# Kernel tuning notes

Hardware: AMD Instinct MI355X
Metric: run time of the kernel (lower is better)

Reference implementation:

```python
import jax, jax.numpy as jnp
import numpy as np


def setup_inputs() -> dict:
    key = jax.random.key(0)
    k1, k2 = jax.random.split(key)
    T, D, K = 100000, 768, 500  # frames, feature dim (HuBERT base), k-means clusters
    feat = jax.random.normal(k1, (T, D), dtype=jnp.float32)
    C = jax.random.normal(k2, (D, K), dtype=jnp.float32)  # cluster centers, transposed as in module
    return {"feat": feat, "C": C}


def reference(feat, C):
    # Squared euclidean distance expanded: ||f||^2 - 2 f.C + ||c||^2
    Cnorm = jnp.sum(C * C, axis=0, keepdims=True)            # [1, K]
    fnorm = jnp.sum(feat * feat, axis=1, keepdims=True)       # [T, 1]
    dist = fnorm - 2.0 * jnp.matmul(feat, C) + Cnorm          # [T, K]
    return jnp.argmin(dist, axis=1)[None, :]                  # [1, T] cluster ids
```

## Files before the change

kernel.cpp:

```cpp
#include <hip/hip_runtime.h>
#include <float.h>

#define D_DIM 768
#define K_DIM 500
#define NDT   24
#define BM    64
#define NTH   256
#define PB_STRIDE 100352

typedef _Float16 f16x8 __attribute__((ext_vector_type(8)));
typedef float    f32x4 __attribute__((ext_vector_type(4)));


__global__ void cnorm_partial_kernel(const float* __restrict__ C,
                                     double* __restrict__ partial, int K) {
    const int k = threadIdx.x;
    const int w = blockIdx.x;
    double s = 0.0;
    if (k < K) {
        const int d0 = w * (D_DIM / 16);
        for (int d = d0; d < d0 + (D_DIM / 16); ++d) {
            const float c = C[(size_t)d * K + k];
            s = fma((double)c, (double)c, s);
        }
    }
    partial[w * 512 + k] = s;
}

__global__ void cnorm_finish_kernel(const double* __restrict__ partial,
                                    float* __restrict__ cnorm, int K) {
    const int k = threadIdx.x;
    if (k < K) {
        double s = 0.0;
        for (int w = 0; w < 16; ++w) s += partial[w * 512 + k];
        cnorm[k] = (float)s;
    } else {
        cnorm[k] = FLT_MAX;
    }
}

__global__ void packB_kernel(const float* __restrict__ C,
                             _Float16* __restrict__ BpH,
                             _Float16* __restrict__ BpL) {
    const int idx = blockIdx.x * 256 + threadIdx.x;
    const int col = idx & 511;
    const int dt  = idx >> 9;
    f16x8 h[4], l[4];
    #pragma unroll
    for (int c = 0; c < 4; ++c)
        #pragma unroll
        for (int j = 0; j < 8; ++j) {
            const int k = c * 8 + j;
            const float v = (col < K_DIM)
                          ? C[(size_t)(dt * 32 + k) * K_DIM + col] : 0.0f;
            const _Float16 hh = (_Float16)v;
            h[c][j] = hh;
            l[c][j] = (_Float16)(v - (float)hh);
        }
    f16x8* dH = (f16x8*)(BpH + ((size_t)dt * 512 + col) * 32);
    f16x8* dL = (f16x8*)(BpL + ((size_t)dt * 512 + col) * 32);
    #pragma unroll
    for (int c = 0; c < 4; ++c) { dH[c] = h[c]; dL[c] = l[c]; }
}

__launch_bounds__(NTH, 3)
__global__ void assign_kernel(const float* __restrict__ feat,
                              const _Float16* __restrict__ BpH,
                              const _Float16* __restrict__ BpL,
                              const float* __restrict__ cnorm,
                              float* __restrict__ pbv,
                              int* __restrict__ pbi,
                              int T) {
    __shared__ __align__(16) _Float16 AsH[2][BM * 32];
    __shared__ __align__(16) _Float16 AsL[2][BM * 32];
    __shared__ float red_v[BM * 4];
    __shared__ int   red_i[BM * 4];

    const int tid  = threadIdx.x;
    const int wn   = tid >> 6;
    const int lane = tid & 63;
    const int l15  = lane & 15;
    const int kg   = lane >> 4;
    const int bid  = blockIdx.x;
    const int half = bid & 1;
    const int R0   = (bid >> 1) * BM;

    const int ar = tid >> 2;
    const int ac = (tid & 3) << 3;
    const bool arow_ok = (R0 + ar) < T;
    const float* fptr = feat + (size_t)(R0 + ar) * D_DIM + ac;
    const int asl = ((ac >> 3) + (ar >> 1)) & 3;

    const int colbase = half * 256 + wn * 64 + l15;
    const _Float16* bpH = BpH + (size_t)colbase * 32 + kg * 8;
    const _Float16* bpL = BpL + (size_t)colbase * 32 + kg * 8;

    f32x4 acc[4][4];
    #pragma unroll
    for (int m = 0; m < 4; ++m)
        #pragma unroll
        for (int n = 0; n < 4; ++n) acc[m][n] = (f32x4){0.f, 0.f, 0.f, 0.f};

    {
        float4 v0 = make_float4(0.f, 0.f, 0.f, 0.f), v1 = v0;
        if (arow_ok) {
            v0 = *(const float4*)(fptr);
            v1 = *(const float4*)(fptr + 4);
        }
        const float fa[8] = {v0.x, v0.y, v0.z, v0.w, v1.x, v1.y, v1.z, v1.w};
        f16x8 h, l;
        #pragma unroll
        for (int j = 0; j < 8; ++j) {
            const _Float16 hh = (_Float16)fa[j];
            h[j] = hh; l[j] = (_Float16)(fa[j] - (float)hh);
        }
        ((f16x8*)AsH[0])[ar * 4 + asl] = h;
        ((f16x8*)AsL[0])[ar * 4 + asl] = l;
    }
    __syncthreads();

    for (int dt = 0; dt < NDT; ++dt) {
        const int cur = dt & 1;
        const bool hasNext = (dt + 1) < NDT;

        f16x8 aH[4], aL[4];
        #pragma unroll
        for (int m = 0; m < 4; ++m) {
            const int row = m * 16 + l15;
            const int sl  = (kg + (row >> 1)) & 3;
            aH[m] = ((const f16x8*)AsH[cur])[row * 4 + sl];
            aL[m] = ((const f16x8*)AsL[cur])[row * 4 + sl];
        }

        const size_t bo = (size_t)dt * 16384;
        f16x8 bH[4], bL[4];
        #pragma unroll
        for (int nh = 0; nh < 4; ++nh) {
            bH[nh] = *(const f16x8*)(bpH + bo + nh * 512);
            bL[nh] = *(const f16x8*)(bpL + bo + nh * 512);
        }

        float4 v0 = make_float4(0.f, 0.f, 0.f, 0.f), v1 = v0;
        if (hasNext && arow_ok) {
            v0 = *(const float4*)(fptr + (dt + 1) * 32);
            v1 = *(const float4*)(fptr + (dt + 1) * 32 + 4);
        }

        #pragma unroll
        for (int nh = 0; nh < 4; ++nh) {
            #pragma unroll
            for (int m = 0; m < 4; ++m) {
                f32x4 a = acc[m][nh];
                a = __builtin_amdgcn_mfma_f32_16x16x32_f16(aH[m], bH[nh], a, 0, 0, 0);
                a = __builtin_amdgcn_mfma_f32_16x16x32_f16(aL[m], bH[nh], a, 0, 0, 0);
                a = __builtin_amdgcn_mfma_f32_16x16x32_f16(aH[m], bL[nh], a, 0, 0, 0);
                acc[m][nh] = a;
            }
        }

        if (hasNext) {
            const float fa[8] = {v0.x, v0.y, v0.z, v0.w, v1.x, v1.y, v1.z, v1.w};
            f16x8 h, l;
            #pragma unroll
            for (int j = 0; j < 8; ++j) {
                const _Float16 hh = (_Float16)fa[j];
                h[j] = hh; l[j] = (_Float16)(fa[j] - (float)hh);
            }
            ((f16x8*)AsH[cur ^ 1])[ar * 4 + asl] = h;
            ((f16x8*)AsL[cur ^ 1])[ar * 4 + asl] = l;
        }
        __syncthreads();
    }

    float cn[4];
    #pragma unroll
    for (int nh = 0; nh < 4; ++nh)
        cn[nh] = cnorm[half * 256 + wn * 64 + nh * 16 + l15];

    #pragma unroll
    for (int m = 0; m < 4; ++m) {
        #pragma unroll
        for (int r = 0; r < 4; ++r) {
            float best = cn[0] - 2.0f * acc[m][0][r];
            int   bi   = colbase;
            #pragma unroll
            for (int nh = 1; nh < 4; ++nh) {
                const int col = colbase + nh * 16;
                const float s = cn[nh] - 2.0f * acc[m][nh][r];
                if (s < best || (s == best && col < bi)) { best = s; bi = col; }
            }
            #pragma unroll
            for (int msk = 1; msk < 16; msk <<= 1) {
                const float ov = __shfl_xor(best, msk, 64);
                const int   oi = __shfl_xor(bi,   msk, 64);
                if (ov < best || (ov == best && oi < bi)) { best = ov; bi = oi; }
            }
            if (l15 == 0) {
                const int rl = m * 16 + kg * 4 + r;
                red_v[rl * 4 + wn] = best;
                red_i[rl * 4 + wn] = bi;
            }
        }
    }
    __syncthreads();

    if (tid < BM) {
        float bv = red_v[tid * 4];
        int   bi = red_i[tid * 4];
        #pragma unroll
        for (int w = 1; w < 4; ++w) {
            const float v = red_v[tid * 4 + w];
            const int   i = red_i[tid * 4 + w];
            if (v < bv || (v == bv && i < bi)) { bv = v; bi = i; }
        }
        const int r = R0 + tid;
        if (r < T) {
            pbv[(size_t)half * PB_STRIDE + r] = bv;
            pbi[(size_t)half * PB_STRIDE + r] = bi;
        }
    }
}

__global__ void combine_kernel(const float* __restrict__ pbv,
                               const int* __restrict__ pbi,
                               int* __restrict__ out, int T) {
    const int r = blockIdx.x * 256 + threadIdx.x;
    if (r < T) {
        const float s0 = pbv[r];
        const int   i0 = pbi[r];
        const float s1 = pbv[PB_STRIDE + r];
        const int   i1 = pbi[PB_STRIDE + r];
        out[r] = (s1 < s0) ? i1 : i0;
    }
}

extern "C" void kernel_launch(void* const* d_in, const int* in_sizes, int n_in,
                              void* d_out, int out_size, void* d_ws, size_t ws_size,
                              hipStream_t stream) {
    const float* feat = (const float*)d_in[0];
    const float* C    = (const float*)d_in[1];
    int* out          = (int*)d_out;
    const int T = in_sizes[0] / D_DIM;
    const int K = in_sizes[1] / D_DIM;

    float*     cnorm   = (float*)d_ws;
    double*    partial = (double*)((char*)d_ws + 4096);
    _Float16*  BpH     = (_Float16*)((char*)d_ws + 131072);
    _Float16*  BpL     = (_Float16*)((char*)d_ws + 917504);
    float*     pbv     = (float*)((char*)d_ws + 1703936);
    int*       pbi     = (int*)((char*)d_ws + 2506752);

    hipLaunchKernelGGL(cnorm_partial_kernel, dim3(16), dim3(512), 0, stream,
                       C, partial, K);
    hipLaunchKernelGGL(cnorm_finish_kernel, dim3(1), dim3(512), 0, stream,
                       partial, cnorm, K);
    hipLaunchKernelGGL(packB_kernel, dim3(48), dim3(256), 0, stream,
                       C, BpH, BpL);

    const int nrb = (T + BM - 1) / BM;
    hipLaunchKernelGGL(assign_kernel, dim3(nrb * 2), dim3(NTH), 0, stream,
                       feat, BpH, BpL, cnorm, pbv, pbi, T);
    hipLaunchKernelGGL(combine_kernel, dim3((T + 255) / 256), dim3(256), 0, stream,
                       pbv, pbi, out, T);
}
```

Baseline: 272.2 us.

## Switch split-fp16 GEMM to 32x32x16 MFMA tiles with raised issue priority

Replaces the 16x16x32 MFMA tiling (4x4 accumulators of 4 floats) with 32x32x16 MFMA tiles (2x2 accumulators of 16 floats) and remaps the LDS A-fragment and global B-fragment loads to match the new operand layout. The larger tiles need fewer LDS and global fragment loads per FLOP and fewer MFMA instructions. The argmin epilogue is rewritten for the 32-lane column layout and the new output row mapping. s_setprio is raised around the MFMA block to favour matrix-instruction issue across waves. The change risks register pressure at 3 waves per SIMD and depends on the row-index remapping being correct.

```diff
diff --git a/kernel.cpp b/kernel.cpp
--- a/kernel.cpp
+++ b/kernel.cpp
@@ -8,8 +8,8 @@
 #define NTH   256
 #define PB_STRIDE 100352
 
-typedef _Float16 f16x8 __attribute__((ext_vector_type(8)));
-typedef float    f32x4 __attribute__((ext_vector_type(4)));
+typedef _Float16 f16x8  __attribute__((ext_vector_type(8)));
+typedef float    f32x16 __attribute__((ext_vector_type(16)));
 
 
 __global__ void cnorm_partial_kernel(const float* __restrict__ C,
@@ -79,8 +79,8 @@
     const int tid  = threadIdx.x;
     const int wn   = tid >> 6;
     const int lane = tid & 63;
-    const int l15  = lane & 15;
-    const int kg   = lane >> 4;
+    const int c5   = lane & 31;
+    const int kh   = lane >> 5;
     const int bid  = blockIdx.x;
     const int half = bid & 1;
     const int R0   = (bid >> 1) * BM;
@@ -91,15 +91,17 @@
     const float* fptr = feat + (size_t)(R0 + ar) * D_DIM + ac;
     const int asl = ((ac >> 3) + (ar >> 1)) & 3;
 
-    const int colbase = half * 256 + wn * 64 + l15;
-    const _Float16* bpH = BpH + (size_t)colbase * 32 + kg * 8;
-    const _Float16* bpL = BpL + (size_t)colbase * 32 + kg * 8;
-
-    f32x4 acc[4][4];
-    #pragma unroll
-    for (int m = 0; m < 4; ++m)
-        #pragma unroll
-        for (int n = 0; n < 4; ++n) acc[m][n] = (f32x4){0.f, 0.f, 0.f, 0.f};
+    const int colbase = half * 256 + wn * 64 + c5;
+    const _Float16* bpH = BpH + (size_t)colbase * 32 + kh * 8;
+    const _Float16* bpL = BpL + (size_t)colbase * 32 + kh * 8;
+
+    f32x16 acc[2][2];
+    #pragma unroll
+    for (int m = 0; m < 2; ++m)
+        #pragma unroll
+        for (int n = 0; n < 2; ++n)
+            #pragma unroll
+            for (int r = 0; r < 16; ++r) acc[m][n][r] = 0.0f;
 
     {
         float4 v0 = make_float4(0.f, 0.f, 0.f, 0.f), v1 = v0;
@@ -123,22 +125,15 @@
         const int cur = dt & 1;
         const bool hasNext = (dt + 1) < NDT;
 
-        f16x8 aH[4], aL[4];
-        #pragma unroll
-        for (int m = 0; m < 4; ++m) {
-            const int row = m * 16 + l15;
-            const int sl  = (kg + (row >> 1)) & 3;
-            aH[m] = ((const f16x8*)AsH[cur])[row * 4 + sl];
-            aL[m] = ((const f16x8*)AsL[cur])[row * 4 + sl];
-        }
-
         const size_t bo = (size_t)dt * 16384;
-        f16x8 bH[4], bL[4];
-        #pragma unroll
-        for (int nh = 0; nh < 4; ++nh) {
-            bH[nh] = *(const f16x8*)(bpH + bo + nh * 512);
-            bL[nh] = *(const f16x8*)(bpL + bo + nh * 512);
-        }
+        f16x8 bH[2][2], bL[2][2];
+        #pragma unroll
+        for (int n = 0; n < 2; ++n)
+            #pragma unroll
+            for (int step = 0; step < 2; ++step) {
+                bH[n][step] = *(const f16x8*)(bpH + bo + n * 1024 + step * 16);
+                bL[n][step] = *(const f16x8*)(bpL + bo + n * 1024 + step * 16);
+            }
 
         float4 v0 = make_float4(0.f, 0.f, 0.f, 0.f), v1 = v0;
         if (hasNext && arow_ok) {
@@ -146,17 +141,33 @@
             v1 = *(const float4*)(fptr + (dt + 1) * 32 + 4);
         }
 
-        #pragma unroll
-        for (int nh = 0; nh < 4; ++nh) {
-            #pragma unroll
-            for (int m = 0; m < 4; ++m) {
-                f32x4 a = acc[m][nh];
-                a = __builtin_amdgcn_mfma_f32_16x16x32_f16(aH[m], bH[nh], a, 0, 0, 0);
-                a = __builtin_amdgcn_mfma_f32_16x16x32_f16(aL[m], bH[nh], a, 0, 0, 0);
-                a = __builtin_amdgcn_mfma_f32_16x16x32_f16(aH[m], bL[nh], a, 0, 0, 0);
-                acc[m][nh] = a;
-            }
-        }
+        f16x8 aH[2][2], aL[2][2];
+        #pragma unroll
+        for (int m = 0; m < 2; ++m) {
+            const int row = m * 32 + c5;
+            #pragma unroll
+            for (int step = 0; step < 2; ++step) {
+                const int chunk = step * 2 + kh;
+                const int sl = (chunk + (row >> 1)) & 3;
+                aH[m][step] = ((const f16x8*)AsH[cur])[row * 4 + sl];
+                aL[m][step] = ((const f16x8*)AsL[cur])[row * 4 + sl];
+            }
+        }
+
+        __builtin_amdgcn_s_setprio(1);
+        #pragma unroll
+        for (int step = 0; step < 2; ++step)
+            #pragma unroll
+            for (int n = 0; n < 2; ++n)
+                #pragma unroll
+                for (int m = 0; m < 2; ++m) {
+                    f32x16 a = acc[m][n];
+                    a = __builtin_amdgcn_mfma_f32_32x32x16_f16(aH[m][step], bH[n][step], a, 0, 0, 0);
+                    a = __builtin_amdgcn_mfma_f32_32x32x16_f16(aL[m][step], bH[n][step], a, 0, 0, 0);
+                    a = __builtin_amdgcn_mfma_f32_32x32x16_f16(aH[m][step], bL[n][step], a, 0, 0, 0);
+                    acc[m][n] = a;
+                }
+        __builtin_amdgcn_s_setprio(0);
 
         if (hasNext) {
             const float fa[8] = {v0.x, v0.y, v0.z, v0.w, v1.x, v1.y, v1.z, v1.w};
@@ -172,31 +183,30 @@
         __syncthreads();
     }
 
-    float cn[4];
-    #pragma unroll
-    for (int nh = 0; nh < 4; ++nh)
-        cn[nh] = cnorm[half * 256 + wn * 64 + nh * 16 + l15];
-
-    #pragma unroll
-    for (int m = 0; m < 4; ++m) {
-        #pragma unroll
-        for (int r = 0; r < 4; ++r) {
+    float cn[2];
+    #pragma unroll
+    for (int n = 0; n < 2; ++n)
+        cn[n] = cnorm[half * 256 + wn * 64 + n * 32 + c5];
+
+    #pragma unroll
+    for (int m = 0; m < 2; ++m) {
+        #pragma unroll
+        for (int r = 0; r < 16; ++r) {
             float best = cn[0] - 2.0f * acc[m][0][r];
             int   bi   = colbase;
-            #pragma unroll
-            for (int nh = 1; nh < 4; ++nh) {
-                const int col = colbase + nh * 16;
-                const float s = cn[nh] - 2.0f * acc[m][nh][r];
-                if (s < best || (s == best && col < bi)) { best = s; bi = col; }
-            }
-            #pragma unroll
-            for (int msk = 1; msk < 16; msk <<= 1) {
+            {
+                const float s = cn[1] - 2.0f * acc[m][1][r];
+                const int col = colbase + 32;
+                if (s < best) { best = s; bi = col; }
+            }
+            #pragma unroll
+            for (int msk = 1; msk < 32; msk <<= 1) {
                 const float ov = __shfl_xor(best, msk, 64);
                 const int   oi = __shfl_xor(bi,   msk, 64);
                 if (ov < best || (ov == best && oi < bi)) { best = ov; bi = oi; }
             }
-            if (l15 == 0) {
-                const int rl = m * 16 + kg * 4 + r;
+            if (c5 == 0) {
+                const int rl = m * 32 + 4 * kh + (r & 3) + 8 * (r >> 2);
                 red_v[rl * 4 + wn] = best;
                 red_i[rl * 4 + wn] = bi;
             }
```

New measurement: 326.3 us. +19.9%, slower.

## Process two K-slices per loop iteration and raise MFMA wave priority

Applied to the files above, without the earlier changes.

The main loop now covers two 32-wide depth slices per iteration, so there are 12 iterations instead of 24. This halves the number of __syncthreads barriers and issues more global loads before the MFMA work starts. The MFMA blocks are wrapped in s_setprio so waves in their matrix phase are favoured by the scheduler. In exchange, LDS use and the register load from the extra B fragments both roughly double, which may cut occupancy under launch_bounds(256,3).

```diff
diff --git a/kernel.cpp b/kernel.cpp
--- a/kernel.cpp
+++ b/kernel.cpp
@@ -3,7 +3,7 @@
 
 #define D_DIM 768
 #define K_DIM 500
-#define NDT   24
+#define NIT   12
 #define BM    64
 #define NTH   256
 #define PB_STRIDE 100352
@@ -71,8 +71,8 @@
                               float* __restrict__ pbv,
                               int* __restrict__ pbi,
                               int T) {
-    __shared__ __align__(16) _Float16 AsH[2][BM * 32];
-    __shared__ __align__(16) _Float16 AsL[2][BM * 32];
+    __shared__ __align__(16) _Float16 AsH[2][2][BM * 32];
+    __shared__ __align__(16) _Float16 AsL[2][2][BM * 32];
     __shared__ float red_v[BM * 4];
     __shared__ int   red_i[BM * 4];
 
@@ -101,76 +101,112 @@
         #pragma unroll
         for (int n = 0; n < 4; ++n) acc[m][n] = (f32x4){0.f, 0.f, 0.f, 0.f};
 
+#define CVT_STORE(V0, V1, BUF, SUB) do {                                       \
+    const float fa[8] = {(V0).x, (V0).y, (V0).z, (V0).w,                       \
+                         (V1).x, (V1).y, (V1).z, (V1).w};                      \
+    f16x8 h, l;                                                                \
+    _Pragma("unroll")                                                          \
+    for (int j = 0; j < 8; ++j) {                                              \
+        const _Float16 hh = (_Float16)fa[j];                                   \
+        h[j] = hh; l[j] = (_Float16)(fa[j] - (float)hh);                       \
+    }                                                                          \
+    ((f16x8*)AsH[BUF][SUB])[ar * 4 + asl] = h;                                 \
+    ((f16x8*)AsL[BUF][SUB])[ar * 4 + asl] = l;                                 \
+} while (0)
+
     {
-        float4 v0 = make_float4(0.f, 0.f, 0.f, 0.f), v1 = v0;
+        float4 v0 = make_float4(0.f,0.f,0.f,0.f), v1 = v0, v2 = v0, v3 = v0;
         if (arow_ok) {
             v0 = *(const float4*)(fptr);
             v1 = *(const float4*)(fptr + 4);
-        }
-        const float fa[8] = {v0.x, v0.y, v0.z, v0.w, v1.x, v1.y, v1.z, v1.w};
-        f16x8 h, l;
-        #pragma unroll
-        for (int j = 0; j < 8; ++j) {
-            const _Float16 hh = (_Float16)fa[j];
-            h[j] = hh; l[j] = (_Float16)(fa[j] - (float)hh);
-        }
-        ((f16x8*)AsH[0])[ar * 4 + asl] = h;
-        ((f16x8*)AsL[0])[ar * 4 + asl] = l;
+            v2 = *(const float4*)(fptr + 32);
+            v3 = *(const float4*)(fptr + 36);
+        }
+        CVT_STORE(v0, v1, 0, 0);
+        CVT_STORE(v2, v3, 0, 1);
     }
     __syncthreads();
 
-    for (int dt = 0; dt < NDT; ++dt) {
-        const int cur = dt & 1;
-        const bool hasNext = (dt + 1) < NDT;
-
-        f16x8 aH[4], aL[4];
-        #pragma unroll
-        for (int m = 0; m < 4; ++m) {
-            const int row = m * 16 + l15;
-            const int sl  = (kg + (row >> 1)) & 3;
-            aH[m] = ((const f16x8*)AsH[cur])[row * 4 + sl];
-            aL[m] = ((const f16x8*)AsL[cur])[row * 4 + sl];
-        }
-
-        const size_t bo = (size_t)dt * 16384;
-        f16x8 bH[4], bL[4];
+    for (int it = 0; it < NIT; ++it) {
+        const int cur = it & 1;
+        const bool hasNext = (it + 1) < NIT;
+
+        const size_t bo0 = (size_t)(2 * it) * 16384;
+        const size_t bo1 = bo0 + 16384;
+        f16x8 b0H[4], b0L[4], b1H[4], b1L[4];
         #pragma unroll
         for (int nh = 0; nh < 4; ++nh) {
-            bH[nh] = *(const f16x8*)(bpH + bo + nh * 512);
-            bL[nh] = *(const f16x8*)(bpL + bo + nh * 512);
-        }
-
-        float4 v0 = make_float4(0.f, 0.f, 0.f, 0.f), v1 = v0;
+            b0H[nh] = *(const f16x8*)(bpH + bo0 + nh * 512);
+            b0L[nh] = *(const f16x8*)(bpL + bo0 + nh * 512);
+        }
+        #pragma unroll
+        for (int nh = 0; nh < 4; ++nh) {
+            b1H[nh] = *(const f16x8*)(bpH + bo1 + nh * 512);
+            b1L[nh] = *(const f16x8*)(bpL + bo1 + nh * 512);
+        }
+
+        float4 v0 = make_float4(0.f,0.f,0.f,0.f), v1 = v0, v2 = v0, v3 = v0;
         if (hasNext && arow_ok) {
-            v0 = *(const float4*)(fptr + (dt + 1) * 32);
-            v1 = *(const float4*)(fptr + (dt + 1) * 32 + 4);
-        }
-
-        #pragma unroll
-        for (int nh = 0; nh < 4; ++nh) {
+            const float* p = fptr + (it + 1) * 64;
+            v0 = *(const float4*)(p);
+            v1 = *(const float4*)(p + 4);
+            v2 = *(const float4*)(p + 32);
+            v3 = *(const float4*)(p + 36);
+        }
+
+        {
+            f16x8 aH[4], aL[4];
             #pragma unroll
             for (int m = 0; m < 4; ++m) {
-                f32x4 a = acc[m][nh];
-                a = __builtin_amdgcn_mfma_f32_16x16x32_f16(aH[m], bH[nh], a, 0, 0, 0);
-                a = __builtin_amdgcn_mfma_f32_16x16x32_f16(aL[m], bH[nh], a, 0, 0, 0);
-                a = __builtin_amdgcn_mfma_f32_16x16x32_f16(aH[m], bL[nh], a, 0, 0, 0);
-                acc[m][nh] = a;
-            }
+                const int row = m * 16 + l15;
+                const int sl  = (kg + (row >> 1)) & 3;
+                aH[m] = ((const f16x8*)AsH[cur][0])[row * 4 + sl];
+                aL[m] = ((const f16x8*)AsL[cur][0])[row * 4 + sl];
+            }
+            __builtin_amdgcn_s_setprio(1);
+            #pragma unroll
+            for (int nh = 0; nh < 4; ++nh)
+                #pragma unroll
+                for (int m = 0; m < 4; ++m) {
+                    f32x4 a = acc[m][nh];
+                    a = __builtin_amdgcn_mfma_f32_16x16x32_f16(aH[m], b0H[nh], a, 0, 0, 0);
+                    a = __builtin_amdgcn_mfma_f32_16x16x32_f16(aL[m], b0H[nh], a, 0, 0, 0);
+                    a = __builtin_amdgcn_mfma_f32_16x16x32_f16(aH[m], b0L[nh], a, 0, 0, 0);
+                    acc[m][nh] = a;
+                }
+            __builtin_amdgcn_s_setprio(0);
+        }
+
+        {
+            f16x8 aH[4], aL[4];
+            #pragma unroll
+            for (int m = 0; m < 4; ++m) {
+                const int row = m * 16 + l15;
+                const int sl  = (kg + (row >> 1)) & 3;
+                aH[m] = ((const f16x8*)AsH[cur][1])[row * 4 + sl];
+                aL[m] = ((const f16x8*)AsL[cur][1])[row * 4 + sl];
+            }
+            __builtin_amdgcn_s_setprio(1);
+            #pragma unroll
+            for (int nh = 0; nh < 4; ++nh)
+                #pragma unroll
+                for (int m = 0; m < 4; ++m) {
+                    f32x4 a = acc[m][nh];
+                    a = __builtin_amdgcn_mfma_f32_16x16x32_f16(aH[m], b1H[nh], a, 0, 0, 0);
+                    a = __builtin_amdgcn_mfma_f32_16x16x32_f16(aL[m], b1H[nh], a, 0, 0, 0);
+                    a = __builtin_amdgcn_mfma_f32_16x16x32_f16(aH[m], b1L[nh], a, 0, 0, 0);
+                    acc[m][nh] = a;
+                }
+            __builtin_amdgcn_s_setprio(0);
         }
 
         if (hasNext) {
-            const float fa[8] = {v0.x, v0.y, v0.z, v0.w, v1.x, v1.y, v1.z, v1.w};
-            f16x8 h, l;
-            #pragma unroll
-            for (int j = 0; j < 8; ++j) {
-                const _Float16 hh = (_Float16)fa[j];
-                h[j] = hh; l[j] = (_Float16)(fa[j] - (float)hh);
-            }
-            ((f16x8*)AsH[cur ^ 1])[ar * 4 + asl] = h;
-            ((f16x8*)AsL[cur ^ 1])[ar * 4 + asl] = l;
+            CVT_STORE(v0, v1, cur ^ 1, 0);
+            CVT_STORE(v2, v3, cur ^ 1, 1);
         }
         __syncthreads();
     }
+#undef CVT_STORE
 
     float cn[4];
     #pragma unroll
```

Measured after the change: 429.1 us. +57.6%, slower.

## Prefetch feature tiles two steps ahead and raise wave priority around MFMAs

Applied to the files above, without the earlier changes.

The main loop is unrolled by two with ping-pong register buffers, so global loads of feature data are issued two D-tiles ahead instead of one, giving them more time to land before conversion. B loads are hoisted ahead of the LDS reads of A, and s_setprio brackets the MFMA block to favour waves issuing matrix ops. This costs extra registers for the second prefetch buffer, which may reduce occupancy.

```diff
diff --git a/kernel.cpp b/kernel.cpp
--- a/kernel.cpp
+++ b/kernel.cpp
@@ -101,76 +101,86 @@
         #pragma unroll
         for (int n = 0; n < 4; ++n) acc[m][n] = (f32x4){0.f, 0.f, 0.f, 0.f};
 
+#define CVT_STORE(V0, V1, BUF) do {                                            \
+    const float fa[8] = {(V0).x, (V0).y, (V0).z, (V0).w,                       \
+                         (V1).x, (V1).y, (V1).z, (V1).w};                      \
+    f16x8 h, l;                                                                \
+    _Pragma("unroll")                                                          \
+    for (int j = 0; j < 8; ++j) {                                              \
+        const _Float16 hh = (_Float16)fa[j];                                   \
+        h[j] = hh; l[j] = (_Float16)(fa[j] - (float)hh);                       \
+    }                                                                          \
+    ((f16x8*)AsH[BUF])[ar * 4 + asl] = h;                                      \
+    ((f16x8*)AsL[BUF])[ar * 4 + asl] = l;                                      \
+} while (0)
+
+#define BODY(DT, CUR0, CUR1, NXT0, NXT1) do {                                  \
+    const int cur = (DT) & 1;                                                  \
+      \
+                                       \
+    const size_t bo = (size_t)(DT) * 16384;                                    \
+    f16x8 bH[4], bL[4];                                                        \
+    _Pragma("unroll")                                                          \
+    for (int nh = 0; nh < 4; ++nh) {                                           \
+        bH[nh] = *(const f16x8*)(bpH + bo + nh * 512);                         \
+        bL[nh] = *(const f16x8*)(bpL + bo + nh * 512);                         \
+    }                                                                          \
+             \
+    if ((DT) + 2 < NDT && arow_ok) {                                           \
+        const float* p = fptr + ((DT) + 2) * 32;                               \
+        NXT0 = *(const float4*)(p);                                            \
+        NXT1 = *(const float4*)(p + 4);                                        \
+    }                                                                          \
+                                            \
+    f16x8 aH[4], aL[4];                                                        \
+    _Pragma("unroll")                                                          \
+    for (int m = 0; m < 4; ++m) {                                              \
+        const int row = m * 16 + l15;                                          \
+        const int sl  = (kg + (row >> 1)) & 3;                                 \
+        aH[m] = ((const f16x8*)AsH[cur])[row * 4 + sl];                        \
+        aL[m] = ((const f16x8*)AsL[cur])[row * 4 + sl];                        \
+    }                                                                          \
+    __builtin_amdgcn_s_setprio(1);                                             \
+    _Pragma("unroll")                                                          \
+    for (int nh = 0; nh < 4; ++nh)                                             \
+        _Pragma("unroll")                                                      \
+        for (int m = 0; m < 4; ++m) {                                          \
+            f32x4 a = acc[m][nh];                                              \
+            a = __builtin_amdgcn_mfma_f32_16x16x32_f16(aH[m], bH[nh], a, 0, 0, 0); \
+            a = __builtin_amdgcn_mfma_f32_16x16x32_f16(aL[m], bH[nh], a, 0, 0, 0); \
+            a = __builtin_amdgcn_mfma_f32_16x16x32_f16(aH[m], bL[nh], a, 0, 0, 0); \
+            acc[m][nh] = a;                                                    \
+        }                                                                      \
+    __builtin_amdgcn_s_setprio(0);                                             \
+              \
+    if ((DT) + 1 < NDT) {                                                      \
+        CVT_STORE(CUR0, CUR1, cur ^ 1);                                        \
+    }                                                                          \
+    __syncthreads();                                                           \
+} while (0)
+
     {
         float4 v0 = make_float4(0.f, 0.f, 0.f, 0.f), v1 = v0;
         if (arow_ok) {
             v0 = *(const float4*)(fptr);
             v1 = *(const float4*)(fptr + 4);
         }
-        const float fa[8] = {v0.x, v0.y, v0.z, v0.w, v1.x, v1.y, v1.z, v1.w};
-        f16x8 h, l;
-        #pragma unroll
-        for (int j = 0; j < 8; ++j) {
-            const _Float16 hh = (_Float16)fa[j];
-            h[j] = hh; l[j] = (_Float16)(fa[j] - (float)hh);
-        }
-        ((f16x8*)AsH[0])[ar * 4 + asl] = h;
-        ((f16x8*)AsL[0])[ar * 4 + asl] = l;
+        CVT_STORE(v0, v1, 0);
+    }
+    float4 pa0 = make_float4(0.f, 0.f, 0.f, 0.f), pa1 = pa0;
+    float4 pb0 = pa0, pb1 = pa0;
+    if (arow_ok) {
+        pa0 = *(const float4*)(fptr + 32);
+        pa1 = *(const float4*)(fptr + 36);
     }
     __syncthreads();
 
-    for (int dt = 0; dt < NDT; ++dt) {
-        const int cur = dt & 1;
-        const bool hasNext = (dt + 1) < NDT;
-
-        f16x8 aH[4], aL[4];
-        #pragma unroll
-        for (int m = 0; m < 4; ++m) {
-            const int row = m * 16 + l15;
-            const int sl  = (kg + (row >> 1)) & 3;
-            aH[m] = ((const f16x8*)AsH[cur])[row * 4 + sl];
-            aL[m] = ((const f16x8*)AsL[cur])[row * 4 + sl];
-        }
-
-        const size_t bo = (size_t)dt * 16384;
-        f16x8 bH[4], bL[4];
-        #pragma unroll
-        for (int nh = 0; nh < 4; ++nh) {
-            bH[nh] = *(const f16x8*)(bpH + bo + nh * 512);
-            bL[nh] = *(const f16x8*)(bpL + bo + nh * 512);
-        }
-
-        float4 v0 = make_float4(0.f, 0.f, 0.f, 0.f), v1 = v0;
-        if (hasNext && arow_ok) {
-            v0 = *(const float4*)(fptr + (dt + 1) * 32);
-            v1 = *(const float4*)(fptr + (dt + 1) * 32 + 4);
-        }
-
-        #pragma unroll
-        for (int nh = 0; nh < 4; ++nh) {
-            #pragma unroll
-            for (int m = 0; m < 4; ++m) {
-                f32x4 a = acc[m][nh];
-                a = __builtin_amdgcn_mfma_f32_16x16x32_f16(aH[m], bH[nh], a, 0, 0, 0);
-                a = __builtin_amdgcn_mfma_f32_16x16x32_f16(aL[m], bH[nh], a, 0, 0, 0);
-                a = __builtin_amdgcn_mfma_f32_16x16x32_f16(aH[m], bL[nh], a, 0, 0, 0);
-                acc[m][nh] = a;
-            }
-        }
-
-        if (hasNext) {
-            const float fa[8] = {v0.x, v0.y, v0.z, v0.w, v1.x, v1.y, v1.z, v1.w};
-            f16x8 h, l;
-            #pragma unroll
-            for (int j = 0; j < 8; ++j) {
-                const _Float16 hh = (_Float16)fa[j];
-                h[j] = hh; l[j] = (_Float16)(fa[j] - (float)hh);
-            }
-            ((f16x8*)AsH[cur ^ 1])[ar * 4 + asl] = h;
-            ((f16x8*)AsL[cur ^ 1])[ar * 4 + asl] = l;
-        }
-        __syncthreads();
-    }
+    for (int it2 = 0; it2 < NDT; it2 += 2) {
+        BODY(it2,     pa0, pa1, pb0, pb1);
+        BODY(it2 + 1, pb0, pb1, pa0, pa1);
+    }
+#undef BODY
+#undef CVT_STORE
 
     float cn[4];
     #pragma unroll
```

Result: faster. 265.9 us (-2.3%).
